# Optimization experiments

Measured on AMD Instinct MI355X. Metric: run time of the kernel, lower is better.

The kernel has to match this reference:

```python
import jax, jax.numpy as jnp
import numpy as np

CHUNK = 64  # rows of `a` processed per step to bound the [chunk, N, d] abs-diff intermediate
TAIL_K = 4          # selection_tail_size
FAR_K = 64          # far_sample_count
PUSH_K = 4          # pushing_sample_size
HUBER_DELTA = 1.0   # torch.nn.HuberLoss default


def cdist_l1(a, b):
    # a: [M, d], b: [N, d] -> [M, N] Manhattan distances, computed in row chunks
    M, d = a.shape
    def f(a_chunk):  # [CHUNK, d] -> [CHUNK, N]
        return jnp.abs(a_chunk[:, None, :] - b[None, :, :]).sum(-1)
    return jax.lax.map(f, a.reshape(-1, CHUNK, d)).reshape(M, b.shape[0])


def smallest_k_mean(dists, k):
    # mean of the k smallest entries along last dim
    neg_vals, _ = jax.lax.top_k(-dists, k)
    return (-neg_vals).mean(-1)


def huber(x):
    # HuberLoss(pred=x, target=0), delta=1
    ax = jnp.abs(x)
    return jnp.where(ax < HUBER_DELTA, 0.5 * x * x, HUBER_DELTA * (ax - 0.5 * HUBER_DELTA))


def setup_inputs() -> dict:
    key = jax.random.key(0)
    k1, k2 = jax.random.split(key)
    space_samples = jax.random.normal(k1, (2048, 256), dtype=jnp.float32)
    latents = jax.random.normal(k2, (8192, 256), dtype=jnp.float32)
    return {"space_samples": space_samples, "latents": latents}


def reference(space_samples, latents):
    # space_samples: [M, d] drawn from latent_sampler; latents: [N, d]
    space_dists = cdist_l1(space_samples, latents)            # [M, N]
    tail_dists = smallest_k_mean(space_dists, TAIL_K)          # [M]
    far_inds = jax.lax.top_k(tail_dists, FAR_K)[1]             # [FAR_K]
    far_samples = space_samples[far_inds]                      # [FAR_K, d]
    empty_dists = cdist_l1(far_samples, latents)               # [FAR_K, N]
    close_dists = smallest_k_mean(empty_dists, PUSH_K)         # [FAR_K]
    return huber(close_dists).mean()
```

## Files before the change

kernel.cpp:

```cpp
#include <hip/hip_runtime.h>
#include <hip/hip_bf16.h>


static constexpr int M = 2048;
static constexpr int N = 8192;
static constexpr int KQ = 64;
static constexpr int BKQ = 16;
static constexpr int NSTEP = KQ / BKQ;
static constexpr int ROWS_PER_BLK = 128;
static constexpr int COLS_PER_BLK = 128;
static constexpr int NCHUNK = N / COLS_PER_BLK;
static constexpr int SLD_RED = 68;

static constexpr float QS  = 21.0f;
static constexpr float QB  = 126.0f;
static constexpr float INV_QS = 1.0f / 21.0f;

__device__ __forceinline__ float med3f(float a, float b, float c) {
    return __builtin_amdgcn_fmed3f(a, b, c);
}

__device__ __forceinline__ void ins4(float d, float& s0, float& s1, float& s2, float& s3) {
    float n0 = fminf(s0, d);
    float n1 = med3f(s0, s1, d);
    float n2 = med3f(s1, s2, d);
    float n3 = med3f(s2, s3, d);
    s0 = n0; s1 = n1; s2 = n2; s3 = n3;
}

__device__ __forceinline__ unsigned int sad8(unsigned int a, unsigned int b, unsigned int c) {
#if __has_builtin(__builtin_amdgcn_sad_u8)
    return __builtin_amdgcn_sad_u8(a, b, c);
#else
    unsigned int d;
    asm("v_sad_u8 %0, %1, %2, %3" : "=v"(d) : "v"(a), "v"(b), "v"(c));
    return d;
#endif
}

__device__ __forceinline__ void gll16(const unsigned int* g, unsigned int* l) {
    __builtin_amdgcn_global_load_lds(
        (const __attribute__((address_space(1))) unsigned int*)g,
        (__attribute__((address_space(3))) unsigned int*)l, 16, 0, 0);
}

__device__ __forceinline__ unsigned int quant4(const float4 v) {
    const float y0 = fminf(fmaxf(fmaf(v.x, QS, QB), 0.0f), 255.0f);
    const float y1 = fminf(fmaxf(fmaf(v.y, QS, QB), 0.0f), 255.0f);
    const float y2 = fminf(fmaxf(fmaf(v.z, QS, QB), 0.0f), 255.0f);
    const float y3 = fminf(fmaxf(fmaf(v.w, QS, QB), 0.0f), 255.0f);
    const unsigned int b0 = (unsigned int)(int)rintf(y0);
    const unsigned int b1 = (unsigned int)(int)rintf(y1);
    const unsigned int b2 = (unsigned int)(int)rintf(y2);
    const unsigned int b3 = (unsigned int)(int)rintf(y3);
    return b0 | (b1 << 8) | (b2 << 16) | (b3 << 24);
}

__device__ __forceinline__ float huber_pos(float x) {
    const float ax = __builtin_fabsf(x);
    return (ax < 1.0f) ? (0.5f * x * x) : (ax - 0.5f);
}

__global__ __launch_bounds__(256)
void convert_kernel(const float* __restrict__ A, const float* __restrict__ B,
                    unsigned int* __restrict__ At, unsigned int* __restrict__ Bt) {
    __shared__ unsigned int lt[KQ * 65];
    const int tid = threadIdx.x;
    const bool isB = (blockIdx.x < N / 64);
    const float* src = isB ? B : A;
    unsigned int* dst = isB ? Bt : At;
    const int rows = isB ? N : M;
    const int r0 = (isB ? blockIdx.x : (blockIdx.x - N / 64)) * 64;

#pragma unroll
    for (int it = 0; it < 16; ++it) {
        const int qi = it * 256 + tid;
        const int row = qi >> 6;
        const int kq = qi & 63;
        const float4 v = *(const float4*)&src[(r0 + row) * 256 + 4 * kq];
        lt[kq * 65 + row] = quant4(v);
    }
    __syncthreads();
#pragma unroll
    for (int it = 0; it < 16; ++it) {
        const int wi = it * 256 + tid;
        const int row = wi & 63;
        const int kq = wi >> 6;
        dst[(size_t)kq * rows + r0 + row] = lt[kq * 65 + row];
    }
}

__global__ __launch_bounds__(256, 4)
void dist4_kernel(const unsigned int* __restrict__ At, const unsigned int* __restrict__ Bt,
                  float4* __restrict__ ws_dist) {
    __shared__ __align__(16) char smem[34816];
    unsigned int* tiles = (unsigned int*)smem;
    const int tid = threadIdx.x;
    const int tx = tid & 15;
    const int ty = tid >> 4;
    const int bx = blockIdx.x;
    const int by = blockIdx.y;
    const int rowBase = by * ROWS_PER_BLK;
    const int colBase = bx * COLS_PER_BLK;

    const int sKq = tid >> 5;
    const int sC  = (tid & 31) * 4;

    unsigned int acc[8][8];
#pragma unroll
    for (int i = 0; i < 8; ++i)
#pragma unroll
        for (int j = 0; j < 8; ++j) acc[i][j] = 0u;

    auto STAGE = [&](int t, int bufofs) {
        const int kb = t * BKQ;
        gll16(&At[(kb + sKq) * M + rowBase + sC],     tiles + bufofs + sKq * 128 + sC);
        gll16(&At[(kb + sKq + 8) * M + rowBase + sC], tiles + bufofs + (sKq + 8) * 128 + sC);
        gll16(&Bt[(kb + sKq) * N + colBase + sC],     tiles + bufofs + 2048 + sKq * 128 + sC);
        gll16(&Bt[(kb + sKq + 8) * N + colBase + sC], tiles + bufofs + 2048 + (sKq + 8) * 128 + sC);
    };

    auto LDQ = [&](const unsigned int* As, const unsigned int* Bs, int kq,
                   uint4& a0, uint4& a1, uint4& b0, uint4& b1) {
        a0 = *(const uint4*)&As[kq * 128 + 8 * ty];
        a1 = *(const uint4*)&As[kq * 128 + 8 * ty + 4];
        b0 = *(const uint4*)&Bs[kq * 128 + 4 * tx];
        b1 = *(const uint4*)&Bs[kq * 128 + 64 + 4 * tx];
    };

    auto SADQ = [&](const uint4& aw0, const uint4& aw1, const uint4& bw0, const uint4& bw1) {
        const unsigned int a[8] = {aw0.x, aw0.y, aw0.z, aw0.w, aw1.x, aw1.y, aw1.z, aw1.w};
        const unsigned int b[8] = {bw0.x, bw0.y, bw0.z, bw0.w, bw1.x, bw1.y, bw1.z, bw1.w};
#pragma unroll
        for (int i = 0; i < 8; ++i)
#pragma unroll
            for (int j = 0; j < 8; ++j)
                acc[i][j] = sad8(a[i], b[j], acc[i][j]);
    };

    STAGE(0, 0);

    for (int t0 = 0; t0 < NSTEP; ++t0) {
        __syncthreads();
        if (t0 + 1 < NSTEP) STAGE(t0 + 1, ((t0 + 1) & 1) * 4096);

        const unsigned int* As = tiles + (t0 & 1) * 4096;
        const unsigned int* Bs = As + 2048;

        uint4 eA0, eA1, eB0, eB1, oA0, oA1, oB0, oB1;
        LDQ(As, Bs, 0, eA0, eA1, eB0, eB1);
#pragma unroll
        for (int h = 0; h < 8; ++h) {
            LDQ(As, Bs, 2 * h + 1, oA0, oA1, oB0, oB1);
            SADQ(eA0, eA1, eB0, eB1);
            if (h < 7) LDQ(As, Bs, 2 * h + 2, eA0, eA1, eB0, eB1);
            SADQ(oA0, oA1, oB0, oB1);
        }
    }

    float s[8][4];
#pragma unroll
    for (int i = 0; i < 8; ++i) {
        float s0 = 1e30f, s1 = 1e30f, s2 = 1e30f, s3 = 1e30f;
#pragma unroll
        for (int j = 0; j < 8; ++j) {
            const float d = (float)acc[i][j] * INV_QS;
            ins4(d, s0, s1, s2, s3);
        }
        s[i][0] = s0; s[i][1] = s1; s[i][2] = s2; s[i][3] = s3;
    }

    __syncthreads();
    float (*red)[SLD_RED] = (float (*)[SLD_RED])smem;
#pragma unroll
    for (int i = 0; i < 8; ++i) {
        *(float4*)&red[8 * ty + i][4 * tx] = make_float4(s[i][0], s[i][1], s[i][2], s[i][3]);
    }
    __syncthreads();

    if (tid < ROWS_PER_BLK) {
        float s0 = 1e30f, s1 = 1e30f, s2 = 1e30f, s3 = 1e30f;
#pragma unroll
        for (int c = 0; c < 16; ++c) {
            const float4 v = *(const float4*)&red[tid][4 * c];
            ins4(v.x, s0, s1, s2, s3);
            ins4(v.y, s0, s1, s2, s3);
            ins4(v.z, s0, s1, s2, s3);
            ins4(v.w, s0, s1, s2, s3);
        }
        ws_dist[bx * M + rowBase + tid] = make_float4(s0, s1, s2, s3);
    }
}

__global__ __launch_bounds__(256)
void tail_kernel(const float4* __restrict__ ws_dist, float* __restrict__ tail) {
    const int gtid = blockIdx.x * 256 + threadIdx.x;
    const int row = gtid >> 3;
    const int q = gtid & 7;
    float s0 = 1e30f, s1 = 1e30f, s2 = 1e30f, s3 = 1e30f;
#pragma unroll
    for (int c = 0; c < 8; ++c) {
        const float4 v = ws_dist[(q * 8 + c) * M + row];
        ins4(v.x, s0, s1, s2, s3);
        ins4(v.y, s0, s1, s2, s3);
        ins4(v.z, s0, s1, s2, s3);
        ins4(v.w, s0, s1, s2, s3);
    }
#pragma unroll
    for (int lvl = 1; lvl <= 4; lvl <<= 1) {
        const float o0 = __shfl_xor(s0, lvl, 64);
        const float o1 = __shfl_xor(s1, lvl, 64);
        const float o2 = __shfl_xor(s2, lvl, 64);
        const float o3 = __shfl_xor(s3, lvl, 64);
        ins4(o0, s0, s1, s2, s3);
        ins4(o1, s0, s1, s2, s3);
        ins4(o2, s0, s1, s2, s3);
        ins4(o3, s0, s1, s2, s3);
    }
    if (q == 0) tail[row] = (s0 + s1 + s2 + s3) * 0.25f;
}

__global__ __launch_bounds__(1024)
void top64_kernel(const float* __restrict__ tail, float* __restrict__ out) {
    __shared__ unsigned int hist[8][256];
    __shared__ unsigned int ctrl[2];
    __shared__ float wsum[16];
    __shared__ unsigned int wcnt[16];
    const int tid = threadIdx.x;
    const int wid = tid >> 6;
    const int lane = tid & 63;

    const unsigned int k0 = __float_as_uint(tail[tid]);
    const unsigned int k1 = __float_as_uint(tail[tid + 1024]);

    if (tid == 0) { ctrl[0] = 0u; ctrl[1] = 64u; }

    for (int p = 0; p < 4; ++p) {
        const int shift = 24 - 8 * p;
        ((unsigned int*)hist)[tid] = 0u;
        ((unsigned int*)hist)[tid + 1024] = 0u;
        __syncthreads();
        const unsigned int prefix = ctrl[0];
        const unsigned int t = ctrl[1];
        bool c0 = true, c1 = true;
        if (p > 0) {
            const int sh8 = shift + 8;
            c0 = ((k0 >> sh8) == (prefix >> sh8));
            c1 = ((k1 >> sh8) == (prefix >> sh8));
        }
        if (c0) atomicAdd(&hist[wid & 7][(k0 >> shift) & 255], 1u);
        if (c1) atomicAdd(&hist[wid & 7][(k1 >> shift) & 255], 1u);
        __syncthreads();
        if (tid < 256) {
            unsigned int h = 0;
#pragma unroll
            for (int r = 0; r < 8; ++r) h += hist[r][tid];
            hist[0][tid] = h;
        }
        __syncthreads();
        if (wid == 0) {
            const unsigned int s4 = hist[0][4 * lane] + hist[0][4 * lane + 1] +
                                    hist[0][4 * lane + 2] + hist[0][4 * lane + 3];
            unsigned int suf = s4;
#pragma unroll
            for (int off = 1; off < 64; off <<= 1) {
                const unsigned int v = __shfl_down(suf, off, 64);
                if (lane + off < 64) suf += v;
            }
            const unsigned long long mask = __ballot(suf >= t);
            const int lstar = 63 - __clzll(mask);
            if (lane == lstar) {
                unsigned int c = suf - s4;
                for (int d = 4 * lstar + 3; d >= 4 * lstar; --d) {
                    const unsigned int cd = hist[0][d];
                    c += cd;
                    if (c >= t) {
                        ctrl[0] = prefix | ((unsigned int)d << shift);
                        ctrl[1] = t - (c - cd);
                        break;
                    }
                }
            }
        }
        __syncthreads();
    }

    const unsigned int T = ctrl[0];
    float sum = 0.0f;
    unsigned int cnt = 0;
    if (k0 > T) { ++cnt; sum += huber_pos(__uint_as_float(k0)); }
    if (k1 > T) { ++cnt; sum += huber_pos(__uint_as_float(k1)); }
#pragma unroll
    for (int off = 32; off > 0; off >>= 1) {
        sum += __shfl_down(sum, off, 64);
        cnt += __shfl_down(cnt, off, 64);
    }
    if (lane == 0) { wsum[wid] = sum; wcnt[wid] = cnt; }
    __syncthreads();
    if (tid == 0) {
        float S = 0.0f;
        unsigned int C = 0;
#pragma unroll
        for (int w = 0; w < 16; ++w) { S += wsum[w]; C += wcnt[w]; }
        const float hT = huber_pos(__uint_as_float(T));
        out[0] = (S + (float)(64u - C) * hT) * (1.0f / 64.0f);
    }
}

extern "C" void kernel_launch(void* const* d_in, const int* in_sizes, int n_in,
                              void* d_out, int out_size, void* d_ws, size_t ws_size,
                              hipStream_t stream) {
    const float* A = (const float*)d_in[0];
    const float* B = (const float*)d_in[1];
    float* out = (float*)d_out;

    unsigned int* Bt = (unsigned int*)d_ws;
    unsigned int* At = (unsigned int*)((char*)d_ws + (size_t)KQ * N * 4);
    float4* ws_dist = (float4*)((char*)d_ws + (size_t)KQ * N * 4 + (size_t)KQ * M * 4);
    float* tail = (float*)((char*)ws_dist + (size_t)NCHUNK * M * sizeof(float4));

    convert_kernel<<<dim3(N / 64 + M / 64), 256, 0, stream>>>(A, B, At, Bt);
    dist4_kernel<<<dim3(NCHUNK, M / ROWS_PER_BLK), 256, 0, stream>>>(At, Bt, ws_dist);
    tail_kernel<<<dim3(M * 8 / 256), 256, 0, stream>>>(ws_dist, tail);
    top64_kernel<<<1, 1024, 0, stream>>>(tail, out);
}
```

Before: 112.0 us.

## Restructure distance kernel to stage full B tile and stream A rows from global

The distance kernel now loads the whole 128-column B tile (all 64 k-quads) into shared memory once, then each wave handles 32 rows. Each lane owns two columns and reads the wave-uniform A values directly from global memory as uint4 loads, replacing the double-buffered 16-step shared-memory pipeline and the 8x8 register tile. The top-4 reduction is rewritten as a two-pass shared-memory scatter followed by per-row segment scans and xor shuffles. This removes per-step barriers and LDS traffic for A, but relies on scalar/cached global loads for A and does more per-element work in the reduction.

Measured after the change: 112.2 us. About the same (+0.2%).

```diff
diff --git a/kernel.cpp b/kernel.cpp
--- a/kernel.cpp
+++ b/kernel.cpp
@@ -5,12 +5,10 @@
 static constexpr int M = 2048;
 static constexpr int N = 8192;
 static constexpr int KQ = 64;
-static constexpr int BKQ = 16;
-static constexpr int NSTEP = KQ / BKQ;
 static constexpr int ROWS_PER_BLK = 128;
 static constexpr int COLS_PER_BLK = 128;
 static constexpr int NCHUNK = N / COLS_PER_BLK;
-static constexpr int SLD_RED = 68;
+static constexpr int SLD_RED = 132;
 
 static constexpr float QS  = 21.0f;
 static constexpr float QB  = 126.0f;
@@ -93,102 +91,92 @@
 __global__ __launch_bounds__(256, 4)
 void dist4_kernel(const unsigned int* __restrict__ At, const unsigned int* __restrict__ Bt,
                   float4* __restrict__ ws_dist) {
-    __shared__ __align__(16) char smem[34816];
-    unsigned int* tiles = (unsigned int*)smem;
+    __shared__ __align__(16) char smem[33792];
+    unsigned int* bt = (unsigned int*)smem;
     const int tid = threadIdx.x;
-    const int tx = tid & 15;
-    const int ty = tid >> 4;
+    const int lane = tid & 63;
+    const int w = __builtin_amdgcn_readfirstlane(tid >> 6);
     const int bx = blockIdx.x;
     const int by = blockIdx.y;
     const int rowBase = by * ROWS_PER_BLK;
     const int colBase = bx * COLS_PER_BLK;
-
-    const int sKq = tid >> 5;
-    const int sC  = (tid & 31) * 4;
-
-    unsigned int acc[8][8];
-#pragma unroll
-    for (int i = 0; i < 8; ++i)
-#pragma unroll
-        for (int j = 0; j < 8; ++j) acc[i][j] = 0u;
-
-    auto STAGE = [&](int t, int bufofs) {
-        const int kb = t * BKQ;
-        gll16(&At[(kb + sKq) * M + rowBase + sC],     tiles + bufofs + sKq * 128 + sC);
-        gll16(&At[(kb + sKq + 8) * M + rowBase + sC], tiles + bufofs + (sKq + 8) * 128 + sC);
-        gll16(&Bt[(kb + sKq) * N + colBase + sC],     tiles + bufofs + 2048 + sKq * 128 + sC);
-        gll16(&Bt[(kb + sKq + 8) * N + colBase + sC], tiles + bufofs + 2048 + (sKq + 8) * 128 + sC);
-    };
-
-    auto LDQ = [&](const unsigned int* As, const unsigned int* Bs, int kq,
-                   uint4& a0, uint4& a1, uint4& b0, uint4& b1) {
-        a0 = *(const uint4*)&As[kq * 128 + 8 * ty];
-        a1 = *(const uint4*)&As[kq * 128 + 8 * ty + 4];
-        b0 = *(const uint4*)&Bs[kq * 128 + 4 * tx];
-        b1 = *(const uint4*)&Bs[kq * 128 + 64 + 4 * tx];
-    };
-
-    auto SADQ = [&](const uint4& aw0, const uint4& aw1, const uint4& bw0, const uint4& bw1) {
-        const unsigned int a[8] = {aw0.x, aw0.y, aw0.z, aw0.w, aw1.x, aw1.y, aw1.z, aw1.w};
-        const unsigned int b[8] = {bw0.x, bw0.y, bw0.z, bw0.w, bw1.x, bw1.y, bw1.z, bw1.w};
-#pragma unroll
-        for (int i = 0; i < 8; ++i)
-#pragma unroll
-            for (int j = 0; j < 8; ++j)
-                acc[i][j] = sad8(a[i], b[j], acc[i][j]);
-    };
-
-    STAGE(0, 0);
-
-    for (int t0 = 0; t0 < NSTEP; ++t0) {
-        __syncthreads();
-        if (t0 + 1 < NSTEP) STAGE(t0 + 1, ((t0 + 1) & 1) * 4096);
-
-        const unsigned int* As = tiles + (t0 & 1) * 4096;
-        const unsigned int* Bs = As + 2048;
-
-        uint4 eA0, eA1, eB0, eB1, oA0, oA1, oB0, oB1;
-        LDQ(As, Bs, 0, eA0, eA1, eB0, eB1);
-#pragma unroll
-        for (int h = 0; h < 8; ++h) {
-            LDQ(As, Bs, 2 * h + 1, oA0, oA1, oB0, oB1);
-            SADQ(eA0, eA1, eB0, eB1);
-            if (h < 7) LDQ(As, Bs, 2 * h + 2, eA0, eA1, eB0, eB1);
-            SADQ(oA0, oA1, oB0, oB1);
-        }
-    }
-
-    float s[8][4];
-#pragma unroll
-    for (int i = 0; i < 8; ++i) {
-        float s0 = 1e30f, s1 = 1e30f, s2 = 1e30f, s3 = 1e30f;
-#pragma unroll
-        for (int j = 0; j < 8; ++j) {
-            const float d = (float)acc[i][j] * INV_QS;
-            ins4(d, s0, s1, s2, s3);
-        }
-        s[i][0] = s0; s[i][1] = s1; s[i][2] = s2; s[i][3] = s3;
-    }
+    const int r0 = rowBase + w * 32;
+
+#pragma unroll
+    for (int it = 0; it < 8; ++it) {
+        const int idx = it * 256 + tid;
+        const int kq = idx >> 5;
+        const int c4 = (idx & 31) * 4;
+        gll16(&Bt[(size_t)kq * N + colBase + c4], bt + idx * 4);
+    }
+
+    unsigned int acc[32][2];
+#pragma unroll
+    for (int r = 0; r < 32; ++r) { acc[r][0] = 0u; acc[r][1] = 0u; }
 
     __syncthreads();
+
+    const unsigned int* __restrict__ Arow = At + r0;
+#pragma unroll 4
+    for (int kq = 0; kq < KQ; ++kq) {
+        const uint2 bb = *(const uint2*)&bt[kq * 128 + 2 * lane];
+        const uint4* __restrict__ pa = (const uint4*)(Arow + (size_t)kq * M);
+#pragma unroll
+        for (int q = 0; q < 8; ++q) {
+            const uint4 av = pa[q];
+            acc[4*q+0][0] = sad8(av.x, bb.x, acc[4*q+0][0]);
+            acc[4*q+0][1] = sad8(av.x, bb.y, acc[4*q+0][1]);
+            acc[4*q+1][0] = sad8(av.y, bb.x, acc[4*q+1][0]);
+            acc[4*q+1][1] = sad8(av.y, bb.y, acc[4*q+1][1]);
+            acc[4*q+2][0] = sad8(av.z, bb.x, acc[4*q+2][0]);
+            acc[4*q+2][1] = sad8(av.z, bb.y, acc[4*q+2][1]);
+            acc[4*q+3][0] = sad8(av.w, bb.x, acc[4*q+3][0]);
+            acc[4*q+3][1] = sad8(av.w, bb.y, acc[4*q+3][1]);
+        }
+    }
+
     float (*red)[SLD_RED] = (float (*)[SLD_RED])smem;
-#pragma unroll
-    for (int i = 0; i < 8; ++i) {
-        *(float4*)&red[8 * ty + i][4 * tx] = make_float4(s[i][0], s[i][1], s[i][2], s[i][3]);
-    }
     __syncthreads();
 
-    if (tid < ROWS_PER_BLK) {
-        float s0 = 1e30f, s1 = 1e30f, s2 = 1e30f, s3 = 1e30f;
-#pragma unroll
-        for (int c = 0; c < 16; ++c) {
-            const float4 v = *(const float4*)&red[tid][4 * c];
-            ins4(v.x, s0, s1, s2, s3);
-            ins4(v.y, s0, s1, s2, s3);
-            ins4(v.z, s0, s1, s2, s3);
-            ins4(v.w, s0, s1, s2, s3);
-        }
-        ws_dist[bx * M + rowBase + tid] = make_float4(s0, s1, s2, s3);
+#pragma unroll
+    for (int p = 0; p < 2; ++p) {
+        if ((w >> 1) == p) {
+            const int rl = (w & 1) * 32;
+#pragma unroll
+            for (int r = 0; r < 32; ++r) {
+                *(float2*)&red[rl + r][2 * lane] =
+                    make_float2((float)acc[r][0] * INV_QS, (float)acc[r][1] * INV_QS);
+            }
+        }
+        __syncthreads();
+        {
+            const int row = tid >> 2;
+            const int seg = tid & 3;
+            float s0 = 1e30f, s1 = 1e30f, s2 = 1e30f, s3 = 1e30f;
+#pragma unroll
+            for (int c = 0; c < 8; ++c) {
+                const float4 v = *(const float4*)&red[row][seg * 4 + c * 16];
+                ins4(v.x, s0, s1, s2, s3);
+                ins4(v.y, s0, s1, s2, s3);
+                ins4(v.z, s0, s1, s2, s3);
+                ins4(v.w, s0, s1, s2, s3);
+            }
+#pragma unroll
+            for (int lvl = 1; lvl <= 2; lvl <<= 1) {
+                const float o0 = __shfl_xor(s0, lvl, 64);
+                const float o1 = __shfl_xor(s1, lvl, 64);
+                const float o2 = __shfl_xor(s2, lvl, 64);
+                const float o3 = __shfl_xor(s3, lvl, 64);
+                ins4(o0, s0, s1, s2, s3);
+                ins4(o1, s0, s1, s2, s3);
+                ins4(o2, s0, s1, s2, s3);
+                ins4(o3, s0, s1, s2, s3);
+            }
+            if (seg == 0) {
+                ws_dist[bx * M + rowBase + p * 64 + row] = make_float4(s0, s1, s2, s3);
+            }
+        }
+        __syncthreads();
     }
 }
 
```
